# Performance work log

Hardware: AMD Instinct MI355X
Metric: run time of the kernel (lower is better)

## Reference

```python
import jax, jax.numpy as jnp
import numpy as np

D_MODEL = 1024
N_HEADS = 16
D_HEAD = 64
SCALE = D_HEAD ** -0.5


def setup_inputs() -> dict:
    key = jax.random.key(0)
    k1, k2, k3 = jax.random.split(key, 3)
    B, N = 4, 2048
    x = jax.random.normal(k1, (B, N, D_MODEL), dtype=jnp.float32)
    # NOTE: original torch module overwrites to_q three times, so q/k/v share ONE projection.
    W_qkv = jax.random.normal(k2, (D_MODEL, N_HEADS * D_HEAD), dtype=jnp.float32) * (D_MODEL ** -0.5)
    W_out = jax.random.normal(k3, (N_HEADS * D_HEAD, D_MODEL), dtype=jnp.float32) * (D_MODEL ** -0.5)
    b_out = jnp.zeros((D_MODEL,), dtype=jnp.float32)
    return {"x": x, "W_qkv": W_qkv, "W_out": W_out, "b_out": b_out}


def reference(x, W_qkv, W_out, b_out):
    B, N, _ = x.shape
    # shared projection (faithful to the to_q bug): q = k = v
    qkv = x @ W_qkv                                   # [B, N, H*D]
    q = qkv.reshape(B, N, N_HEADS, D_HEAD).transpose(0, 2, 1, 3)  # [B, H, N, D]
    k = q
    v = q
    scores = jnp.einsum('bhid,bhjd->bhij', q, k) * SCALE          # [B, H, N, N]
    attn = jax.nn.softmax(scores, axis=-1)
    out = jnp.einsum('bhij,bhjd->bhid', attn, v)                  # [B, H, N, D]
    out = out.transpose(0, 2, 1, 3).reshape(B, N, N_HEADS * D_HEAD)
    return out @ W_out + b_out
```

## Files before the change

kernel.cpp:

```cpp
#include <hip/hip_runtime.h>

typedef float  f32x4  __attribute__((ext_vector_type(4)));
typedef __bf16 bf16x8 __attribute__((ext_vector_type(8)));
typedef __bf16 bf16x4 __attribute__((ext_vector_type(4)));
typedef unsigned short u16x8 __attribute__((ext_vector_type(8)));

__device__ __forceinline__ unsigned short f2bf(float f) {
    unsigned u = __builtin_bit_cast(unsigned, f);
    unsigned r = u + 0x7FFFu + ((u >> 16) & 1u);
    return (unsigned short)(r >> 16);
}

__device__ __forceinline__ f32x4 mfma16(bf16x8 a, bf16x8 b, f32x4 c) {
    return __builtin_amdgcn_mfma_f32_16x16x32_bf16(a, b, c, 0, 0, 0);
}
__device__ __forceinline__ f32x4 mfma16u(u16x8 a, u16x8 b, f32x4 c) {
    return __builtin_amdgcn_mfma_f32_16x16x32_bf16(
        __builtin_bit_cast(bf16x8, a), __builtin_bit_cast(bf16x8, b), c, 0, 0, 0);
}

__device__ __forceinline__ float fexp2(float x) {
    float r;
    asm("v_exp_f32 %0, %1" : "=v"(r) : "v"(x));
    return r;
}

__device__ __forceinline__ void gload16(const void* g, void* l) {
    __builtin_amdgcn_global_load_lds((const __attribute__((address_space(1))) void*)g,
                                     (__attribute__((address_space(3))) void*)l,
                                     16, 0, 0);
}

__global__ __launch_bounds__(256) void cast_transpose2(const float* __restrict__ W0,
                                                       const float* __restrict__ W1,
                                                       __bf16* __restrict__ T0Q,
                                                       __bf16* __restrict__ T1Q) {
    const float* W = blockIdx.z ? W1 : W0;
    __bf16* Wt = blockIdx.z ? T1Q : T0Q;
    __shared__ __bf16 T[64][64];
    const int tid = threadIdx.x;
    const int k0 = blockIdx.y * 64, n0 = blockIdx.x * 64;
#pragma unroll
    for (int c = 0; c < 4; ++c) {
        int idx = c * 256 + tid;
        int kr = idx >> 4, nc = (idx & 15) * 4;
        f32x4 w = *(const f32x4*)&W[(size_t)(k0 + kr) * 1024 + n0 + nc];
        int g = ((nc >> 3) ^ (kr >> 3)) * 8 + (nc & 7);
        bf16x4 pk;
        pk[0] = (__bf16)w[0]; pk[1] = (__bf16)w[1];
        pk[2] = (__bf16)w[2]; pk[3] = (__bf16)w[3];
        *(bf16x4*)&T[kr][g] = pk;
    }
    __syncthreads();
#pragma unroll
    for (int c = 0; c < 2; ++c) {
        int idx = c * 256 + tid;
        int n = idx >> 3, k8 = (idx & 7) * 8;
        bf16x8 o;
#pragma unroll
        for (int e = 0; e < 8; ++e) {
            int k = k8 + e;
            o[e] = T[k][((n >> 3) ^ (k >> 3)) * 8 + (n & 7)];
        }
        *(bf16x8*)&Wt[(size_t)(n0 + n) * 1024 + k0 + k8] = o;
    }
}

template <bool OUT_BF16, bool WRITE_VT, bool CAST_A>
__global__ __launch_bounds__(256) void gemm_bt(const void* __restrict__ Av,
                                               const unsigned short* __restrict__ Bt,
                                               void* __restrict__ Cout,
                                               const float* __restrict__ bias,
                                               __bf16* __restrict__ vT) {
    constexpr int K = 1024, NN = 1024;
    __shared__ unsigned short SM[16384];
    const int tid  = threadIdx.x;
    const int lane = tid & 63, wid = tid >> 6;
    const int wm = wid >> 1, wn = wid & 1;
    const int i = lane & 15, qg = lane >> 4;
    const int bid = blockIdx.y * 8 + blockIdx.x;
    const int swz = (bid & 7) * 64 + (bid >> 3);
    const int tm = (swz >> 3) * 128, tn = (swz & 7) * 128;

    const int rl  = wid * 32 + (lane >> 3);
    const int gsw = ((lane & 7) ^ (rl & 7)) * 8;
    const unsigned short* Bsrc = &Bt[(size_t)(tn + rl) * K + gsw];
    const unsigned short* Asrc = &((const unsigned short*)Av)[(size_t)(tm + rl) * K + gsw];
    const int srow = tid >> 3, scol = (tid & 7) * 8;
    const float* Afsrc = &((const float*)Av)[(size_t)(tm + srow) * K + scol];
    const int acol = ((scol >> 3) ^ (srow & 7)) * 8;

    f32x4 acc[4][4] = {};

    auto STAGE = [&]() {
#pragma unroll
        for (int c = 0; c < 4; ++c) {
            if constexpr (CAST_A) {
                int row = c * 32 + srow;
                const float* p = Afsrc + (size_t)c * 32 * K;
                f32x4 a0 = *(const f32x4*)p;
                f32x4 a1 = *(const f32x4*)(p + 4);
                u16x8 av;
                av[0] = f2bf(a0[0]); av[1] = f2bf(a0[1]);
                av[2] = f2bf(a0[2]); av[3] = f2bf(a0[3]);
                av[4] = f2bf(a1[0]); av[5] = f2bf(a1[1]);
                av[6] = f2bf(a1[2]); av[7] = f2bf(a1[3]);
                *(u16x8*)&SM[row * 64 + acol] = av;
            } else {
                gload16(Asrc + (size_t)c * 8 * K, &SM[(wid * 32 + c * 8) * 64]);
            }
            gload16(Bsrc + (size_t)c * 8 * K, &SM[8192 + (wid * 32 + c * 8) * 64]);
        }
        Afsrc += 64; Asrc += 64; Bsrc += 64;
    };

    auto COMP = [&]() {
        const unsigned short* As = SM;
        const unsigned short* Bs = SM + 8192;
#pragma unroll
        for (int ks = 0; ks < 2; ++ks) {
            u16x8 af[4], bfr[4];
#pragma unroll
            for (int m = 0; m < 4; ++m)
                af[m]  = *(const u16x8*)&As[(wm * 64 + m * 16 + i) * 64 + (((ks * 4 + qg) ^ (i & 7)) * 8)];
#pragma unroll
            for (int nn = 0; nn < 4; ++nn)
                bfr[nn] = *(const u16x8*)&Bs[(wn * 64 + nn * 16 + i) * 64 + (((ks * 4 + qg) ^ (i & 7)) * 8)];
#pragma unroll
            for (int m = 0; m < 4; ++m)
#pragma unroll
                for (int nn = 0; nn < 4; ++nn)
                    acc[m][nn] = mfma16u(af[m], bfr[nn], acc[m][nn]);
        }
    };

    for (int kk = 0; kk < 16; ++kk) {
        STAGE();
        __syncthreads();
        COMP();
        __syncthreads();
    }

    const int r0 = qg * 4;
#pragma unroll
    for (int nn = 0; nn < 4; ++nn) {
        int col = tn + wn * 64 + nn * 16 + i;
        float bv = 0.f;
        if constexpr (!OUT_BF16) bv = bias[col];
#pragma unroll
        for (int m = 0; m < 4; ++m) {
            int rowb = tm + wm * 64 + m * 16 + r0;
#pragma unroll
            for (int r = 0; r < 4; ++r) {
                if constexpr (OUT_BF16)
                    ((unsigned short*)Cout)[(size_t)(rowb + r) * NN + col] = f2bf(acc[m][nn][r]);
                else
                    ((float*)Cout)[(size_t)(rowb + r) * NN + col] = acc[m][nn][r] + bv;
            }
        }
    }

    if constexpr (WRITE_VT) {
        unsigned short* T = SM;
#pragma unroll
        for (int nn = 0; nn < 4; ++nn) {
            const int col = wn * 64 + nn * 16 + i;
            const int g = col >> 3, c7 = col & 7;
#pragma unroll
            for (int m = 0; m < 4; ++m) {
                const int rbase = wm * 64 + m * 16 + r0;
                const int rsw = (rbase >> 3) & 15;
#pragma unroll
                for (int r = 0; r < 4; ++r)
                    T[(rbase + r) * 128 + ((g ^ rsw) * 8) + c7] = f2bf(acc[m][nn][r]);
            }
        }
        __syncthreads();
        const size_t vb0 = ((size_t)(tm >> 11) * 16 + (tn >> 6)) * 131072 + (size_t)(tm & 2047);
#pragma unroll
        for (int c = 0; c < 8; ++c) {
            int idx = c * 256 + tid;
            int hh = idx >> 10, dd = (idx >> 4) & 63, n8 = (idx & 15) * 8;
            int g = (hh * 64 + dd) >> 3, c7 = dd & 7, rsw = idx & 15;
            u16x8 o;
#pragma unroll
            for (int e = 0; e < 8; ++e)
                o[e] = T[(n8 + e) * 128 + ((g ^ rsw) * 8) + c7];
            *(u16x8*)&vT[vb0 + (size_t)hh * 131072 + (size_t)dd * 2048 + n8] = o;
        }
    }
}

__global__ __launch_bounds__(256, 4) void flash_attn9(const __bf16* __restrict__ qkv,
                                                      const __bf16* __restrict__ vT,
                                                      __bf16* __restrict__ attnout) {
    __shared__ __bf16 Ks[2][4096];
    __shared__ __bf16 Vs[2][4096];

    const int tid = threadIdx.x, lane = tid & 63, wid = tid >> 6;
    const int i = lane & 15, qg = lane >> 4;

    const int n = blockIdx.x;
    const int j = n & 7, t = n >> 3;
    const int head = j * 8 + (t >> 4);
    const int b = head >> 4, h = head & 15;
    const int q0 = (t & 15) * 128;

    const size_t base  = (size_t)b * (2048 * 1024) + (size_t)h * 64;
    const size_t vbase = (size_t)head * (64 * 2048);

    const float SL2E = 0.18033688f;

    bf16x8 qf[2][2];
#pragma unroll
    for (int g = 0; g < 2; ++g) {
        int qrow = q0 + wid * 32 + g * 16 + i;
#pragma unroll
        for (int s = 0; s < 2; ++s) {
            bf16x8 tq = *(const bf16x8*)&qkv[base + (size_t)qrow * 1024 + s * 32 + qg * 8];
#pragma unroll
            for (int e = 0; e < 8; ++e)
                qf[g][s][e] = (__bf16)((float)tq[e] * SL2E);
        }
    }

    const int r0s = tid >> 3, g0s = tid & 7;
    const __bf16* ksrc0 = &qkv[base + (size_t)r0s * 1024 + (size_t)((g0s ^ (r0s & 7)) * 8)];
    const __bf16* ksrc1 = ksrc0 + 32 * 1024;
    const __bf16* vsrc0 = &vT[vbase + (size_t)r0s * 2048 + (size_t)((g0s ^ (r0s & 7)) * 8)];
    const __bf16* vsrc1 = vsrc0 + 32 * 2048;

    auto STAGE = [&](int buf) {
        gload16(ksrc0, &Ks[buf][wid * 512]);
        gload16(ksrc1, &Ks[buf][2048 + wid * 512]);
        gload16(vsrc0, &Vs[buf][wid * 512]);
        gload16(vsrc1, &Vs[buf][2048 + wid * 512]);
        ksrc0 += 64 * 1024; ksrc1 += 64 * 1024;
        vsrc0 += 64;        vsrc1 += 64;
    };

    f32x4 po[2][4] = {};
    f32x4 po5[2]   = {};
    bf16x8 ones;
#pragma unroll
    for (int e = 0; e < 8; ++e) ones[e] = (__bf16)1.0f;

    auto BODY = [&](const __bf16* Kb, const __bf16* Vb) {
        __builtin_amdgcn_s_setprio(1);
        f32x4 st[2][4];
#pragma unroll
        for (int m = 0; m < 4; ++m) {
            bf16x8 kf0 = *(const bf16x8*)&Kb[(m * 16 + i) * 64 + ((qg) ^ (i & 7)) * 8];
            bf16x8 kf1 = *(const bf16x8*)&Kb[(m * 16 + i) * 64 + ((4 + qg) ^ (i & 7)) * 8];
            f32x4 z0 = {}, z1 = {};
            z0 = mfma16(kf0, qf[0][0], z0);
            st[0][m] = mfma16(kf1, qf[0][1], z0);
            z1 = mfma16(kf0, qf[1][0], z1);
            st[1][m] = mfma16(kf1, qf[1][1], z1);
        }
        __builtin_amdgcn_s_setprio(0);

        bf16x8 pa[2][2];
#pragma unroll
        for (int g = 0; g < 2; ++g) {
#pragma unroll
            for (int m = 0; m < 4; ++m)
#pragma unroll
                for (int r = 0; r < 4; ++r)
                    st[g][m][r] = fexp2(st[g][m][r]);

#pragma unroll
            for (int r = 0; r < 4; ++r) {
                pa[g][0][r]     = (__bf16)st[g][0][r];
                pa[g][0][4 + r] = (__bf16)st[g][1][r];
                pa[g][1][r]     = (__bf16)st[g][2][r];
                pa[g][1][4 + r] = (__bf16)st[g][3][r];
            }
        }

        __builtin_amdgcn_s_setprio(1);
#pragma unroll
        for (int s = 0; s < 2; ++s) {
#pragma unroll
            for (int nf = 0; nf < 4; ++nf) {
                const int row = nf * 16 + i;
                bf16x8 vf;
                *(bf16x4*)&vf = *(const bf16x4*)
                    &Vb[row * 64 + (((s * 4 + (qg >> 1)) ^ (i & 7)) * 8 + (qg & 1) * 4)];
                *((bf16x4*)&vf + 1) = *(const bf16x4*)
                    &Vb[row * 64 + (((s * 4 + 2 + (qg >> 1)) ^ (i & 7)) * 8 + (qg & 1) * 4)];
                po[0][nf] = mfma16(pa[0][s], vf, po[0][nf]);
                po[1][nf] = mfma16(pa[1][s], vf, po[1][nf]);
            }
            po5[0] = mfma16(pa[0][s], ones, po5[0]);
            po5[1] = mfma16(pa[1][s], ones, po5[1]);
        }
        __builtin_amdgcn_s_setprio(0);
    };

    STAGE(0);
    __syncthreads();
    for (int kt2 = 0; kt2 < 16; ++kt2) {
        STAGE(1);
        BODY(Ks[0], Vs[0]);
        __syncthreads();
        if (kt2 < 15) STAGE(0);
        BODY(Ks[1], Vs[1]);
        __syncthreads();
    }

#pragma unroll
    for (int g = 0; g < 2; ++g) {
        float linv[4];
#pragma unroll
        for (int r = 0; r < 4; ++r) linv[r] = __builtin_amdgcn_rcpf(po5[g][r]);
#pragma unroll
        for (int nf = 0; nf < 4; ++nf)
#pragma unroll
            for (int r = 0; r < 4; ++r) {
                int row = q0 + wid * 32 + g * 16 + qg * 4 + r;
                attnout[base + (size_t)row * 1024 + nf * 16 + i] = (__bf16)(po[g][nf][r] * linv[r]);
            }
    }
}

extern "C" void kernel_launch(void* const* d_in, const int* in_sizes, int n_in,
                              void* d_out, int out_size, void* d_ws, size_t ws_size,
                              hipStream_t stream) {
    const float* x    = (const float*)d_in[0];
    const float* Wqkv = (const float*)d_in[1];
    const float* Wout = (const float*)d_in[2];
    const float* bout = (const float*)d_in[3];
    float* out = (float*)d_out;

    char* ws = (char*)d_ws;
    unsigned short* aout = (unsigned short*)(ws);
    unsigned short* qkvb = (unsigned short*)(ws + (16u << 20));
    __bf16*         vTp  = (__bf16*)(ws + (32u << 20));
    __bf16*         wqt  = (__bf16*)(ws + (48u << 20));
    __bf16*         wot  = (__bf16*)(ws + (50u << 20));

    cast_transpose2<<<dim3(16, 16, 2), 256, 0, stream>>>(Wqkv, Wout, wqt, wot);

    gemm_bt<true, true, true><<<dim3(8, 64), 256, 0, stream>>>(x, (const unsigned short*)wqt,
                                                               qkvb, nullptr, vTp);

    flash_attn9<<<1024, 256, 0, stream>>>((const __bf16*)qkvb, vTp, (__bf16*)aout);

    gemm_bt<false, false, false><<<dim3(8, 64), 256, 0, stream>>>(aout, (const unsigned short*)wot,
                                                                  out, bout, nullptr);
}
```

Before: 140.7 us.

## Double-buffer GEMM LDS tiles to overlap global loads with MFMA compute

Doubles the shared-memory allocation to two tile buffers and prefetches the next K-slice (async B/A loads, or fp32 A held in registers before the bf16 cast) while the MFMAs run on the current buffer. This removes one barrier per iteration and hides global-load latency behind compute. The cost is twice the LDS (64KB per block), which may reduce occupancy, plus extra registers for the prefetched A values.

```diff
diff --git a/kernel.cpp b/kernel.cpp
--- a/kernel.cpp
+++ b/kernel.cpp
@@ -73,7 +73,7 @@
                                                const float* __restrict__ bias,
                                                __bf16* __restrict__ vT) {
     constexpr int K = 1024, NN = 1024;
-    __shared__ unsigned short SM[16384];
+    __shared__ unsigned short SM[32768];
     const int tid  = threadIdx.x;
     const int lane = tid & 63, wid = tid >> 6;
     const int wm = wid >> 1, wn = wid & 1;
@@ -91,32 +91,42 @@
     const int acol = ((scol >> 3) ^ (srow & 7)) * 8;
 
     f32x4 acc[4][4] = {};
-
-    auto STAGE = [&]() {
+    f32x4 areg[4][2];
+
+    auto LOADA = [&](int t) {
 #pragma unroll
         for (int c = 0; c < 4; ++c) {
-            if constexpr (CAST_A) {
-                int row = c * 32 + srow;
-                const float* p = Afsrc + (size_t)c * 32 * K;
-                f32x4 a0 = *(const f32x4*)p;
-                f32x4 a1 = *(const f32x4*)(p + 4);
-                u16x8 av;
-                av[0] = f2bf(a0[0]); av[1] = f2bf(a0[1]);
-                av[2] = f2bf(a0[2]); av[3] = f2bf(a0[3]);
-                av[4] = f2bf(a1[0]); av[5] = f2bf(a1[1]);
-                av[6] = f2bf(a1[2]); av[7] = f2bf(a1[3]);
-                *(u16x8*)&SM[row * 64 + acol] = av;
-            } else {
-                gload16(Asrc + (size_t)c * 8 * K, &SM[(wid * 32 + c * 8) * 64]);
-            }
-            gload16(Bsrc + (size_t)c * 8 * K, &SM[8192 + (wid * 32 + c * 8) * 64]);
-        }
-        Afsrc += 64; Asrc += 64; Bsrc += 64;
-    };
-
-    auto COMP = [&]() {
-        const unsigned short* As = SM;
-        const unsigned short* Bs = SM + 8192;
+            const float* p = Afsrc + (size_t)t * 64 + (size_t)c * 32 * K;
+            areg[c][0] = *(const f32x4*)p;
+            areg[c][1] = *(const f32x4*)(p + 4);
+        }
+    };
+    auto WRITEA = [&](int buf) {
+        unsigned short* dst = &SM[buf * 16384];
+#pragma unroll
+        for (int c = 0; c < 4; ++c) {
+            u16x8 av;
+            av[0] = f2bf(areg[c][0][0]); av[1] = f2bf(areg[c][0][1]);
+            av[2] = f2bf(areg[c][0][2]); av[3] = f2bf(areg[c][0][3]);
+            av[4] = f2bf(areg[c][1][0]); av[5] = f2bf(areg[c][1][1]);
+            av[6] = f2bf(areg[c][1][2]); av[7] = f2bf(areg[c][1][3]);
+            *(u16x8*)&dst[(c * 32 + srow) * 64 + acol] = av;
+        }
+    };
+    auto STAGE = [&](int t, int buf) {
+        unsigned short* dst = &SM[buf * 16384];
+        if constexpr (!CAST_A) {
+#pragma unroll
+            for (int c = 0; c < 4; ++c)
+                gload16(Asrc + (size_t)t * 64 + (size_t)c * 8 * K, &dst[(wid * 32 + c * 8) * 64]);
+        }
+#pragma unroll
+        for (int c = 0; c < 4; ++c)
+            gload16(Bsrc + (size_t)t * 64 + (size_t)c * 8 * K, &dst[8192 + (wid * 32 + c * 8) * 64]);
+    };
+    auto COMP = [&](int buf) {
+        const unsigned short* As = &SM[buf * 16384];
+        const unsigned short* Bs = As + 8192;
 #pragma unroll
         for (int ks = 0; ks < 2; ++ks) {
             u16x8 af[4], bfr[4];
@@ -134,10 +144,19 @@
         }
     };
 
+    if constexpr (CAST_A) LOADA(0);
+    STAGE(0, 0);
+    if constexpr (CAST_A) WRITEA(0);
+    __syncthreads();
     for (int kk = 0; kk < 16; ++kk) {
-        STAGE();
-        __syncthreads();
-        COMP();
+        if (kk < 15) {
+            if constexpr (CAST_A) LOADA(kk + 1);
+            STAGE(kk + 1, (kk + 1) & 1);
+        }
+        COMP(kk & 1);
+        if (kk < 15) {
+            if constexpr (CAST_A) WRITEA((kk + 1) & 1);
+        }
         __syncthreads();
     }
 
```

New measurement: 136.9 us. 1.03x faster.
